# Performance work log

Measured on AMD Instinct MI355X. Metric: run time of the kernel, lower is better.

Reference implementation:

```python
import jax, jax.numpy as jnp
import numpy as np

NUM_BRANCH = 4
KERNEL_SIZES = (1, 3, 5, 7)
NUM_CLASSES = 1000
IN_C = 256
OUT_C = 256


def _cond_conv(x, w, emb, y):
    # x: [B,C,H,W], w: [O,I,k,k], emb: [num_classes,O], y: [B]
    out = jax.lax.conv_general_dilated(
        x, w, window_strides=(1, 1), padding='SAME',
        dimension_numbers=('NCHW', 'OIHW', 'NCHW'))
    return out + emb[y][:, :, None, None]


def setup_inputs() -> dict:
    key = jax.random.key(0)
    ks = jax.random.split(key, 2 + 2 * NUM_BRANCH)
    B, H = 64, 32
    inp = {
        'x': jax.random.normal(ks[0], (B, IN_C, H, H), dtype=jnp.float32),
        'y': jax.random.randint(ks[1], (B,), 0, NUM_CLASSES, dtype=jnp.int64),
        'sample_arc': jax.random.randint(jax.random.fold_in(key, 7), (B,), 0, NUM_BRANCH, dtype=jnp.int64),
    }
    for i, k in enumerate(KERNEL_SIZES):
        fan_in = IN_C * k * k
        inp[f'w{i}'] = jax.random.normal(ks[2 + 2 * i], (OUT_C, IN_C, k, k), dtype=jnp.float32) / np.sqrt(fan_in)
        inp[f'e{i}'] = jax.random.normal(ks[3 + 2 * i], (NUM_CLASSES, OUT_C), dtype=jnp.float32) * 0.02
    return inp


def reference(x, y, sample_arc, w0, w1, w2, w3, e0, e1, e2, e3):
    ws = (w0, w1, w2, w3)
    es = (e0, e1, e2, e3)
    # Compute every branch for every sample (as the original module does),
    # stack along branch dim: [B, num_branch, O, H, W]
    branch_out = jnp.stack([_cond_conv(x, w, e, y) for w, e in zip(ws, es)], axis=1)
    onehot = jax.nn.one_hot(sample_arc, NUM_BRANCH, dtype=x.dtype)  # [B, num_branch]
    # mask-and-sum (one-hot multiply then reduce over branch dim)
    return jnp.einsum('bn,bnchw->bchw', onehot, branch_out)
```

## Files before the change

kernel.cpp:

```cpp
#include <hip/hip_runtime.h>


typedef unsigned short ushort_t;
typedef __attribute__((ext_vector_type(8))) short short8;
typedef __attribute__((ext_vector_type(4))) float f32x4;

#define CIN   256
#define COUT  256
#define HH    32
#define WW    32
#define HW    1024

#define XT_ELEMS   16777216
#define WT_OFF_0   0
#define WT_OFF_1   65536
#define WT_OFF_2   655360
#define WT_OFF_3   2293760
#define WT_ELEMS   5505024
#define TILE_BYTE_OFF ((size_t)(XT_ELEMS + WT_ELEMS) * 2)
#define MAX_TILES  2048
#define WS_NEEDED  (TILE_BYTE_OFF + MAX_TILES * 2 + 64)

#define XS_R_STRIDE 1216
#define XS_ELEMS    12160

__device__ inline ushort_t f2bf(float f) {
    unsigned x = __builtin_bit_cast(unsigned, f);
    unsigned r = (x + 0x7FFFu + ((x >> 16) & 1u)) >> 16;
    return (ushort_t)r;
}

__device__ inline void gld16(const ushort_t* g, ushort_t* l) {
    __builtin_amdgcn_global_load_lds(
        (const __attribute__((address_space(1))) unsigned int*)g,
        (__attribute__((address_space(3))) unsigned int*)l, 16, 0, 0);
}

__global__ __launch_bounds__(256) void prep_kernel(
    const float* __restrict__ x,
    const float* __restrict__ w0, const float* __restrict__ w1,
    const float* __restrict__ w2, const float* __restrict__ w3,
    const int* __restrict__ arc,
    ushort_t* __restrict__ xt, ushort_t* __restrict__ wt,
    ushort_t* __restrict__ tiles, unsigned* __restrict__ cnt) {
    __shared__ float lds[2 * 32 * 49];
    const int blk = blockIdx.x;
    const int tid = threadIdx.x;

    if (blk < 4096) {
        const int a   = blk >> 10;
        const int cc  = (blk >> 7) & 7;
        const int oc0 = (blk & 127) * 2;
        const int kk  = (a == 0) ? 1 : (a == 1) ? 9 : (a == 2) ? 25 : 49;
        const float* __restrict__ w = (a == 0) ? w0 : (a == 1) ? w1
                                    : (a == 2) ? w2 : w3;
        const size_t woff = (a == 0) ? WT_OFF_0 : (a == 1) ? WT_OFF_1
                          : (a == 2) ? WT_OFF_2 : WT_OFF_3;
        const int ckk = 32 * kk;
#pragma unroll
        for (int ocq = 0; ocq < 2; ++ocq) {
            const float* src = w + ((size_t)((oc0 + ocq) * CIN + cc * 32)) * kk;
            for (int i = tid; i < ckk; i += 256) lds[ocq * ckk + i] = src[i];
        }
        __syncthreads();
        ushort_t* dst = wt + woff + ((size_t)(cc * COUT + oc0)) * kk * 32;
        const int F = 2 * kk * 32;
        for (int j = tid; j < F; j += 256) {
            const int ci  = j & 31;
            const int t2  = j >> 5;
            const int khw = t2 % kk;
            const int ocq = t2 / kk;
            dst[j] = f2bf(lds[ocq * ckk + ci * kk + khw]);
        }
    } else if (blk < 12288) {
        const int g  = (blk - 4096) * 256 + tid;
        const int q8 = g & 3;
        const int hw = (g >> 2) & 1023;
        const int cc = (g >> 12) & 7;
        const int b  = g >> 15;
        const float* src = x + ((size_t)(b * CIN + cc * 32 + q8 * 8)) * HW + hw;
        short8 o;
#pragma unroll
        for (int j = 0; j < 8; ++j)
            o[j] = (short)f2bf(src[(size_t)j * HW]);
        *(short8*)(xt + (size_t)g * 8) = o;
    } else if (tid < 64) {
        const int lane = tid;
        const int ab = (int)arc[lane];
        unsigned long long m[4];
#pragma unroll
        for (int v = 0; v < 4; ++v) m[v] = __ballot(ab == v);
        int gt = 0;
#pragma unroll
        for (int v = 1; v < 4; ++v) if (v > ab) gt += __popcll(m[v]);
        const unsigned long long eq = (ab == 0) ? m[0] : (ab == 1) ? m[1]
                                    : (ab == 2) ? m[2] : m[3];
        const unsigned long long lower = (lane == 0) ? 0ull
                                       : (~0ull >> (64 - lane));
        const int rank = gt + __popcll(eq & lower);
        const int nh   = __popcll(m[2]) + __popcll(m[3]);
        const bool heavy = (ab >= 2);
        const int myCnt = heavy ? 32 : 16;
        const int start = heavy ? 32 * rank : 32 * nh + 16 * (rank - nh);
        for (int j = 0; j < myCnt; ++j)
            tiles[start + j] = (ushort_t)((lane << 5) | j);
        if (lane == 0) { cnt[0] = 0u; cnt[1] = (unsigned)(1024 + 16 * nh); }
    }
}

template <int K, int MT>
__device__ void conv_body(const ushort_t* __restrict__ xt,
                          const ushort_t* __restrict__ wtb,
                          const float* __restrict__ eb,
                          int b, int cls, int oc0, int r0,
                          float* __restrict__ out, ushort_t* xs) {
    constexpr int KK  = K * K;
    constexpr int PAD = K / 2;
    constexpr int R   = 4 + 2 * PAD;

    const int tid  = threadIdx.x;
    const int wave = tid >> 6;
    const int lane = tid & 63;
    const int wm   = wave >> 1;
    const int wn   = wave & 1;
    const int ln   = lane & 15;
    const int q    = lane >> 4;

    f32x4 acc[MT][4];
#pragma unroll
    for (int mt = 0; mt < MT; ++mt)
#pragma unroll
        for (int nt = 0; nt < 4; ++nt) acc[mt][nt] = (f32x4)0.0f;

    const int ocw = oc0 + wm * (MT * 16);
    const ushort_t* wcol = wtb + ((size_t)(ocw + ln) * KK) * 32 + q * 8;
    short8 afp[MT];
#pragma unroll
    for (int mt = 0; mt < MT; ++mt)
        afp[mt] = *(const short8*)&wcol[(size_t)(mt * 16 * KK) * 32];

    const ushort_t* xsrc = xt + ((size_t)b * 8) * (HW * 32);

    for (int cc = 0; cc < 8; ++cc) {
        __syncthreads();
#pragma unroll
        for (int i = 0; i < R / 2; ++i) {
            const int run = i * 4 + wave;
            const int r   = run >> 1;
            const int h   = run & 1;
            const int gr  = r0 - PAD + r;
            ushort_t* ldst = xs + r * XS_R_STRIDE + 96 + h * 512;
            if (gr >= 0 && gr < HH) {
                const ushort_t* src =
                    xsrc + ((size_t)(cc * HW + gr * WW)) * 32 + h * 512 + lane * 8;
                gld16(src, ldst);
            } else {
                *(short8*)(ldst + lane * 8) = (short8)0;
            }
        }
        __syncthreads();

        const ushort_t* wb = wcol + ((size_t)cc * COUT * KK) * 32;
#pragma unroll 1
        for (int kh = 0; kh < K; ++kh) {
#pragma unroll
            for (int kw = 0; kw < K; ++kw) {
                const int khw = kh * K + kw;
                short8 afc[MT];
#pragma unroll
                for (int mt = 0; mt < MT; ++mt) afc[mt] = afp[mt];
                {
                    int nkhw = khw + 1;
                    const ushort_t* nb = wb;
                    if (nkhw == KK) {
                        nkhw = 0;
                        if (cc < 7) nb = wb + ((size_t)COUT * KK) * 32;
                    }
#pragma unroll
                    for (int mt = 0; mt < MT; ++mt)
                        afp[mt] = *(const short8*)&nb[(size_t)(mt * 16 * KK + nkhw) * 32];
                }
                short8 bf[4];
#pragma unroll
                for (int nt = 0; nt < 4; ++nt) {
                    const int rl = wn * 2 + (nt >> 1) + kh;
                    const int c  = (nt & 1) * 16 + ln + 3 + (kw - PAD);
                    bf[nt] = *(const short8*)&xs[rl * XS_R_STRIDE + c * 32 + q * 8];
                }
#pragma unroll
                for (int mt = 0; mt < MT; ++mt)
#pragma unroll
                    for (int nt = 0; nt < 4; ++nt)
                        acc[mt][nt] = __builtin_amdgcn_mfma_f32_16x16x32_bf16(
                            afc[mt], bf[nt], acc[mt][nt], 0, 0, 0);
            }
        }
    }

#pragma unroll
    for (int mt = 0; mt < MT; ++mt) {
#pragma unroll
        for (int i = 0; i < 4; ++i) {
            const int oc = ocw + mt * 16 + q * 4 + i;
            const float ev = eb[(size_t)cls * COUT + oc];
            float* ob = out + ((size_t)(b * COUT + oc)) * HW;
#pragma unroll
            for (int nt = 0; nt < 4; ++nt) {
                const int row = r0 + wn * 2 + (nt >> 1);
                const int col = (nt & 1) * 16 + ln;
                ob[row * WW + col] = acc[mt][nt][i] + ev;
            }
        }
    }
}

__global__ __launch_bounds__(256, 4) void conv_mfma(
    const ushort_t* __restrict__ xt, const ushort_t* __restrict__ wt,
    const int* __restrict__ y, const int* __restrict__ arc,
    const float* __restrict__ e0, const float* __restrict__ e1,
    const float* __restrict__ e2, const float* __restrict__ e3,
    float* __restrict__ out,
    const ushort_t* __restrict__ tiles, unsigned* __restrict__ cnt) {
    __shared__ ushort_t xs[XS_ELEMS];
    __shared__ int t_sh;
    const int tid = threadIdx.x;
    const unsigned T = cnt[1];

    for (int i = tid; i < 240; i += 256) {
        const int g    = i & 3;
        const int cell = i >> 2;
        const int cidx = cell % 6;
        const int r    = cell / 6;
        const int col  = (cidx < 3) ? cidx : cidx + 32;
        *(short8*)&xs[r * XS_R_STRIDE + col * 32 + g * 8] = (short8)0;
    }

    for (;;) {
        if (tid == 0) {
            const unsigned t = atomicAdd(cnt, 1u);
            t_sh = (t < T) ? (int)tiles[t] : -1;
        }
        __syncthreads();
        const int e = t_sh;
        __syncthreads();
        if (e < 0) break;

        const int b   = e >> 5;
        const int j   = e & 31;
        const int a   = __builtin_amdgcn_readfirstlane(arc[b]);
        const int cls = __builtin_amdgcn_readfirstlane(y[b]);
        switch (a) {
            case 0:  conv_body<1, 4>(xt, wt + WT_OFF_0, e0, b, cls,
                                     (j & 1) << 7, (j >> 1) << 2, out, xs); break;
            case 1:  conv_body<3, 4>(xt, wt + WT_OFF_1, e1, b, cls,
                                     (j & 1) << 7, (j >> 1) << 2, out, xs); break;
            case 2:  conv_body<5, 2>(xt, wt + WT_OFF_2, e2, b, cls,
                                     (j & 3) << 6, (j >> 2) << 2, out, xs); break;
            default: conv_body<7, 2>(xt, wt + WT_OFF_3, e3, b, cls,
                                     (j & 3) << 6, (j >> 2) << 2, out, xs); break;
        }
    }
}

__global__ __launch_bounds__(256) void cond_conv_direct(
    const float* __restrict__ x, const int* __restrict__ y,
    const int* __restrict__ arc,
    const float* __restrict__ w0, const float* __restrict__ e0,
    const float* __restrict__ w1, const float* __restrict__ e1,
    const float* __restrict__ w2, const float* __restrict__ e2,
    const float* __restrict__ w3, const float* __restrict__ e3,
    float* __restrict__ out) {
    const int b   = blockIdx.x >> 4;
    const int o0  = (blockIdx.x & 15) << 4;
    const int tid = threadIdx.x;
    const int col  = tid & 31;
    const int row0 = tid >> 5;
    int a   = __builtin_amdgcn_readfirstlane(arc[b]);
    int cls = __builtin_amdgcn_readfirstlane(y[b]);
    const int k   = (a == 0) ? 1 : (a == 1) ? 3 : (a == 2) ? 5 : 7;
    const int kk  = k * k;
    const int pad = k >> 1;
    const float* __restrict__ wp = (a == 0) ? w0 : (a == 1) ? w1 : (a == 2) ? w2 : w3;
    const float* __restrict__ ep = (a == 0) ? e0 : (a == 1) ? e1 : (a == 2) ? e2 : e3;
    __shared__ float xsh[8 * HW];
    float acc[16][4];
#pragma unroll
    for (int o = 0; o < 16; ++o)
#pragma unroll
        for (int p = 0; p < 4; ++p) acc[o][p] = 0.f;
    const float* xb = x + (size_t)b * CIN * HW;
    for (int c0 = 0; c0 < CIN; c0 += 8) {
        __syncthreads();
        const float4* src = (const float4*)(xb + c0 * HW);
        float4* dst = (float4*)xsh;
#pragma unroll
        for (int i = 0; i < 8; ++i) dst[tid + (i << 8)] = src[tid + (i << 8)];
        __syncthreads();
        for (int kh = 0; kh < k; ++kh) {
            const int dh = kh - pad;
            int raddr[4]; bool rok[4];
#pragma unroll
            for (int p = 0; p < 4; ++p) {
                const int rr = row0 + 8 * p + dh;
                rok[p] = (rr >= 0) && (rr < HH);
                raddr[p] = (rok[p] ? rr : 0) * WW;
            }
            for (int kw = 0; kw < k; ++kw) {
                const int cc2 = col + kw - pad;
                const bool cok = (cc2 >= 0) && (cc2 < WW);
                const int cofs = cok ? cc2 : 0;
                const int khw = kh * k + kw;
#pragma unroll
                for (int ci = 0; ci < 8; ++ci) {
                    float xv[4];
#pragma unroll
                    for (int p = 0; p < 4; ++p) {
                        const float v = xsh[ci * HW + raddr[p] + cofs];
                        xv[p] = (rok[p] && cok) ? v : 0.f;
                    }
                    const float* wb = wp + (size_t)o0 * CIN * kk + (size_t)(c0 + ci) * kk + khw;
#pragma unroll
                    for (int o = 0; o < 16; ++o) {
                        const float wsv = wb[(size_t)o * CIN * kk];
#pragma unroll
                        for (int p = 0; p < 4; ++p) acc[o][p] += wsv * xv[p];
                    }
                }
            }
        }
    }
    const float* erow = ep + (size_t)cls * COUT + o0;
    float* ob = out + (size_t)(b * COUT + o0) * HW;
#pragma unroll
    for (int o = 0; o < 16; ++o) {
        const float ev = erow[o];
#pragma unroll
        for (int p = 0; p < 4; ++p)
            ob[o * HW + (row0 + 8 * p) * WW + col] = acc[o][p] + ev;
    }
}

extern "C" void kernel_launch(void* const* d_in, const int* in_sizes, int n_in,
                              void* d_out, int out_size, void* d_ws, size_t ws_size,
                              hipStream_t stream) {
    const float* x   = (const float*)d_in[0];
    const int*   y   = (const int*)  d_in[1];
    const int*   arc = (const int*)  d_in[2];
    const float* w0  = (const float*)d_in[3];
    const float* e0  = (const float*)d_in[4];
    const float* w1  = (const float*)d_in[5];
    const float* e1  = (const float*)d_in[6];
    const float* w2  = (const float*)d_in[7];
    const float* e2  = (const float*)d_in[8];
    const float* w3  = (const float*)d_in[9];
    const float* e3  = (const float*)d_in[10];
    float* out = (float*)d_out;
    const int B = in_sizes[1];

    if (ws_size >= WS_NEEDED && B == 64) {
        ushort_t* xt    = (ushort_t*)d_ws;
        ushort_t* wt    = xt + XT_ELEMS;
        ushort_t* tiles = (ushort_t*)((char*)d_ws + TILE_BYTE_OFF);
        unsigned* cnt   = (unsigned*)((char*)d_ws + TILE_BYTE_OFF + MAX_TILES * 2);
        hipLaunchKernelGGL(prep_kernel, dim3(12289), dim3(256), 0, stream,
                           x, w0, w1, w2, w3, arc, xt, wt, tiles, cnt);
        hipLaunchKernelGGL(conv_mfma, dim3(1024), dim3(256), 0, stream,
                           xt, wt, y, arc, e0, e1, e2, e3, out, tiles, cnt);
    } else {
        hipLaunchKernelGGL(cond_conv_direct, dim3(B * 16), dim3(256), 0, stream,
                           x, y, arc, w0, e0, w1, e1, w2, e2, w3, e3, out);
    }
}
```

Baseline: 421.8 us.

## Double-buffer LDS staging, swizzle x layout, retile heavy branches, coalesce x transpose

```diff
diff --git a/kernel.cpp b/kernel.cpp
--- a/kernel.cpp
+++ b/kernel.cpp
@@ -22,7 +22,7 @@
 #define WS_NEEDED  (TILE_BYTE_OFF + MAX_TILES * 2 + 64)
 
 #define XS_R_STRIDE 1216
-#define XS_ELEMS    12160
+#define XS_BUF_ELEMS 9728
 
 __device__ inline ushort_t f2bf(float f) {
     unsigned x = __builtin_bit_cast(unsigned, f);
@@ -43,7 +43,7 @@
     const int* __restrict__ arc,
     ushort_t* __restrict__ xt, ushort_t* __restrict__ wt,
     ushort_t* __restrict__ tiles, unsigned* __restrict__ cnt) {
-    __shared__ float lds[2 * 32 * 49];
+    __shared__ float lds[32 * 258];
     const int blk = blockIdx.x;
     const int tid = threadIdx.x;
 
@@ -72,18 +72,40 @@
             const int ocq = t2 / kk;
             dst[j] = f2bf(lds[ocq * ckk + ci * kk + khw]);
         }
-    } else if (blk < 12288) {
-        const int g  = (blk - 4096) * 256 + tid;
-        const int q8 = g & 3;
-        const int hw = (g >> 2) & 1023;
-        const int cc = (g >> 12) & 7;
-        const int b  = g >> 15;
-        const float* src = x + ((size_t)(b * CIN + cc * 32 + q8 * 8)) * HW + hw;
-        short8 o;
-#pragma unroll
-        for (int j = 0; j < 8; ++j)
-            o[j] = (short)f2bf(src[(size_t)j * HW]);
-        *(short8*)(xt + (size_t)g * 8) = o;
+    } else if (blk < 4608) {
+        const int pxb = blk - 4096;
+        const int b   = pxb >> 3;
+        const int cc  = pxb & 7;
+        const float4* xf4 = (const float4*)x;
+        for (int chunk = 0; chunk < 4; ++chunk) {
+#pragma unroll
+            for (int i = 0; i < 8; ++i) {
+                const int idx = i * 256 + tid;
+                const int ci  = idx >> 6;
+                const int p4  = idx & 63;
+                float4 f = xf4[((size_t)(b * CIN + cc * 32 + ci)) * 256
+                               + chunk * 64 + p4];
+                *(float2*)&lds[ci * 258 + p4 * 4]     = make_float2(f.x, f.y);
+                *(float2*)&lds[ci * 258 + p4 * 4 + 2] = make_float2(f.z, f.w);
+            }
+            __syncthreads();
+#pragma unroll
+            for (int i = 0; i < 4; ++i) {
+                const int g = i * 256 + tid;
+                const int t = g & 3;
+                const int p = g >> 2;
+                const int w_  = p & 31;
+                const int s   = (w_ >> 1) & 3;
+                const int cib = ((t ^ s) << 3);
+                short8 o;
+#pragma unroll
+                for (int j = 0; j < 8; ++j)
+                    o[j] = (short)f2bf(lds[(cib + j) * 258 + p]);
+                *(short8*)(xt + ((size_t)((b * 8 + cc) * HW + chunk * 256 + p)) * 32
+                              + t * 8) = o;
+            }
+            __syncthreads();
+        }
     } else if (tid < 64) {
         const int lane = tid;
         const int ab = (int)arc[lane];
@@ -108,15 +130,16 @@
     }
 }
 
-template <int K, int MT>
+template <int K, int NF>
 __device__ void conv_body(const ushort_t* __restrict__ xt,
                           const ushort_t* __restrict__ wtb,
                           const float* __restrict__ eb,
                           int b, int cls, int oc0, int r0,
-                          float* __restrict__ out, ushort_t* xs) {
+                          float* __restrict__ out,
+                          ushort_t* xs0, ushort_t* xs1) {
     constexpr int KK  = K * K;
     constexpr int PAD = K / 2;
-    constexpr int R   = 4 + 2 * PAD;
+    constexpr int R   = NF + 2 * PAD;
 
     const int tid  = threadIdx.x;
     const int wave = tid >> 6;
@@ -126,39 +149,45 @@
     const int ln   = lane & 15;
     const int q    = lane >> 4;
 
-    f32x4 acc[MT][4];
-#pragma unroll
-    for (int mt = 0; mt < MT; ++mt)
-#pragma unroll
-        for (int nt = 0; nt < 4; ++nt) acc[mt][nt] = (f32x4)0.0f;
-
-    const int ocw = oc0 + wm * (MT * 16);
+    f32x4 acc[4][NF];
+#pragma unroll
+    for (int mt = 0; mt < 4; ++mt)
+#pragma unroll
+        for (int nt = 0; nt < NF; ++nt) acc[mt][nt] = (f32x4)0.0f;
+
+    const int ocw = oc0 + wm * 64;
     const ushort_t* wcol = wtb + ((size_t)(ocw + ln) * KK) * 32 + q * 8;
-    short8 afp[MT];
-#pragma unroll
-    for (int mt = 0; mt < MT; ++mt)
+    short8 afp[4];
+#pragma unroll
+    for (int mt = 0; mt < 4; ++mt)
         afp[mt] = *(const short8*)&wcol[(size_t)(mt * 16 * KK) * 32];
 
     const ushort_t* xsrc = xt + ((size_t)b * 8) * (HW * 32);
 
-    for (int cc = 0; cc < 8; ++cc) {
-        __syncthreads();
+    auto stage = [&](int cc, ushort_t* buf) {
 #pragma unroll
         for (int i = 0; i < R / 2; ++i) {
             const int run = i * 4 + wave;
             const int r   = run >> 1;
             const int h   = run & 1;
             const int gr  = r0 - PAD + r;
-            ushort_t* ldst = xs + r * XS_R_STRIDE + 96 + h * 512;
-            if (gr >= 0 && gr < HH) {
-                const ushort_t* src =
-                    xsrc + ((size_t)(cc * HW + gr * WW)) * 32 + h * 512 + lane * 8;
-                gld16(src, ldst);
-            } else {
+            ushort_t* ldst = buf + r * XS_R_STRIDE + 96 + h * 512;
+            if (gr >= 0 && gr < HH)
+                gld16(xsrc + ((size_t)(cc * HW + gr * WW)) * 32 + h * 512 + lane * 8,
+                      ldst);
+            else
                 *(short8*)(ldst + lane * 8) = (short8)0;
-            }
-        }
-        __syncthreads();
+        }
+    };
+
+    stage(0, xs0);
+
+    for (int cc = 0; cc < 8; ++cc) {
+        ushort_t* cur = (cc & 1) ? xs1 : xs0;
+        ushort_t* nxt = (cc & 1) ? xs0 : xs1;
+        __syncthreads();
+        if (cc < 7) stage(cc + 1, nxt);
+        __builtin_amdgcn_sched_barrier(0);
 
         const ushort_t* wb = wcol + ((size_t)cc * COUT * KK) * 32;
 #pragma unroll 1
@@ -166,9 +195,9 @@
 #pragma unroll
             for (int kw = 0; kw < K; ++kw) {
                 const int khw = kh * K + kw;
-                short8 afc[MT];
-#pragma unroll
-                for (int mt = 0; mt < MT; ++mt) afc[mt] = afp[mt];
+                short8 afc[4];
+#pragma unroll
+                for (int mt = 0; mt < 4; ++mt) afc[mt] = afp[mt];
                 {
                     int nkhw = khw + 1;
                     const ushort_t* nb = wb;
@@ -177,20 +206,24 @@
                         if (cc < 7) nb = wb + ((size_t)COUT * KK) * 32;
                     }
 #pragma unroll
-                    for (int mt = 0; mt < MT; ++mt)
+                    for (int mt = 0; mt < 4; ++mt)
                         afp[mt] = *(const short8*)&nb[(size_t)(mt * 16 * KK + nkhw) * 32];
                 }
-                short8 bf[4];
-#pragma unroll
-                for (int nt = 0; nt < 4; ++nt) {
-                    const int rl = wn * 2 + (nt >> 1) + kh;
-                    const int c  = (nt & 1) * 16 + ln + 3 + (kw - PAD);
-                    bf[nt] = *(const short8*)&xs[rl * XS_R_STRIDE + c * 32 + q * 8];
+                short8 bf[NF];
+#pragma unroll
+                for (int nt = 0; nt < NF; ++nt) {
+                    const int rl = (NF == 4) ? (wn * 2 + (nt >> 1) + kh)
+                                             : (wn + kh);
+                    const int wc = ((NF == 4) ? ((nt & 1) * 16) : (nt * 16))
+                                   + ln + kw - PAD;
+                    const int c    = wc + 3;
+                    const int slot = q ^ ((wc >> 1) & 3);
+                    bf[nt] = *(const short8*)&cur[rl * XS_R_STRIDE + c * 32 + slot * 8];
                 }
 #pragma unroll
-                for (int mt = 0; mt < MT; ++mt)
-#pragma unroll
-                    for (int nt = 0; nt < 4; ++nt)
+                for (int mt = 0; mt < 4; ++mt)
+#pragma unroll
+                    for (int nt = 0; nt < NF; ++nt)
                         acc[mt][nt] = __builtin_amdgcn_mfma_f32_16x16x32_bf16(
                             afc[mt], bf[nt], acc[mt][nt], 0, 0, 0);
             }
@@ -198,16 +231,17 @@
     }
 
 #pragma unroll
-    for (int mt = 0; mt < MT; ++mt) {
+    for (int mt = 0; mt < 4; ++mt) {
 #pragma unroll
         for (int i = 0; i < 4; ++i) {
             const int oc = ocw + mt * 16 + q * 4 + i;
             const float ev = eb[(size_t)cls * COUT + oc];
             float* ob = out + ((size_t)(b * COUT + oc)) * HW;
 #pragma unroll
-            for (int nt = 0; nt < 4; ++nt) {
-                const int row = r0 + wn * 2 + (nt >> 1);
-                const int col = (nt & 1) * 16 + ln;
+            for (int nt = 0; nt < NF; ++nt) {
+                const int row = (NF == 4) ? (r0 + wn * 2 + (nt >> 1))
+                                          : (r0 + wn);
+                const int col = ((NF == 4) ? ((nt & 1) * 16) : (nt * 16)) + ln;
                 ob[row * WW + col] = acc[mt][nt][i] + ev;
             }
         }
@@ -221,18 +255,20 @@
     const float* __restrict__ e2, const float* __restrict__ e3,
     float* __restrict__ out,
     const ushort_t* __restrict__ tiles, unsigned* __restrict__ cnt) {
-    __shared__ ushort_t xs[XS_ELEMS];
+    __shared__ ushort_t xs[2][XS_BUF_ELEMS];
     __shared__ int t_sh;
     const int tid = threadIdx.x;
     const unsigned T = cnt[1];
 
-    for (int i = tid; i < 240; i += 256) {
+    for (int i = tid; i < 384; i += 256) {
         const int g    = i & 3;
         const int cell = i >> 2;
-        const int cidx = cell % 6;
-        const int r    = cell / 6;
+        const int buf  = cell / 48;
+        const int rem  = cell % 48;
+        const int r    = rem / 6;
+        const int cidx = rem % 6;
         const int col  = (cidx < 3) ? cidx : cidx + 32;
-        *(short8*)&xs[r * XS_R_STRIDE + col * 32 + g * 8] = (short8)0;
+        *(short8*)&xs[buf][r * XS_R_STRIDE + col * 32 + g * 8] = (short8)0;
     }
 
     for (;;) {
@@ -247,17 +283,18 @@
 
         const int b   = e >> 5;
         const int j   = e & 31;
+        const int oc0 = (j & 1) << 7;
         const int a   = __builtin_amdgcn_readfirstlane(arc[b]);
         const int cls = __builtin_amdgcn_readfirstlane(y[b]);
         switch (a) {
-            case 0:  conv_body<1, 4>(xt, wt + WT_OFF_0, e0, b, cls,
-                                     (j & 1) << 7, (j >> 1) << 2, out, xs); break;
-            case 1:  conv_body<3, 4>(xt, wt + WT_OFF_1, e1, b, cls,
-                                     (j & 1) << 7, (j >> 1) << 2, out, xs); break;
-            case 2:  conv_body<5, 2>(xt, wt + WT_OFF_2, e2, b, cls,
-                                     (j & 3) << 6, (j >> 2) << 2, out, xs); break;
-            default: conv_body<7, 2>(xt, wt + WT_OFF_3, e3, b, cls,
-                                     (j & 3) << 6, (j >> 2) << 2, out, xs); break;
+            case 0:  conv_body<1, 4>(xt, wt + WT_OFF_0, e0, b, cls, oc0,
+                                     (j >> 1) << 2, out, xs[0], xs[1]); break;
+            case 1:  conv_body<3, 4>(xt, wt + WT_OFF_1, e1, b, cls, oc0,
+                                     (j >> 1) << 2, out, xs[0], xs[1]); break;
+            case 2:  conv_body<5, 2>(xt, wt + WT_OFF_2, e2, b, cls, oc0,
+                                     (j >> 1) << 1, out, xs[0], xs[1]); break;
+            default: conv_body<7, 2>(xt, wt + WT_OFF_3, e3, b, cls, oc0,
+                                     (j >> 1) << 1, out, xs[0], xs[1]); break;
         }
     }
 }
@@ -362,7 +399,7 @@
         ushort_t* wt    = xt + XT_ELEMS;
         ushort_t* tiles = (ushort_t*)((char*)d_ws + TILE_BYTE_OFF);
         unsigned* cnt   = (unsigned*)((char*)d_ws + TILE_BYTE_OFF + MAX_TILES * 2);
-        hipLaunchKernelGGL(prep_kernel, dim3(12289), dim3(256), 0, stream,
+        hipLaunchKernelGGL(prep_kernel, dim3(4609), dim3(256), 0, stream,
                            x, w0, w1, w2, w3, arc, xt, wt, tiles, cnt);
         hipLaunchKernelGGL(conv_mfma, dim3(1024), dim3(256), 0, stream,
                            xt, wt, y, arc, e0, e1, e2, e3, out, tiles, cnt);
```

Measured after the change: 618.5 us. 46.6% more time.
